# Performance work log

Measured on AMD Instinct MI355X. Metric: run time of the kernel, lower is better.

Reference implementation:

```python
import jax, jax.numpy as jnp
import numpy as np

HIDDEN = 512
HEADS = 8
HEAD_SIZE = HIDDEN // HEADS
INF = 10000.0


def _heads(x):
    # [N, L, D] -> [N, L, H, Dh]
    return x.reshape(x.shape[0], x.shape[1], HEADS, HEAD_SIZE)


def _alpha_from_logits(logits, mask_row, mask_col):
    # logits: [N, L1, L2, H]; mask_row: [N, L1]; mask_col: [N, L2]
    pair = (mask_row[:, :, None, None] * mask_col[:, None, :, None]) > 0  # [N,L1,L2,1]
    logits = jnp.where(pair, logits, logits - INF)
    alpha = jax.nn.softmax(logits, axis=2)
    row = (mask_row[:, :, None, None]) > 0  # [N,L1,1,1]
    return jnp.where(row, alpha, jnp.zeros_like(alpha))


def setup_inputs() -> dict:
    key = jax.random.key(0)
    ks = jax.random.split(key, 10)
    N, L1, L2, D = 4, 1024, 1024, HIDDEN
    input1 = jax.random.normal(ks[0], (N, L1, D), dtype=jnp.float32)
    input2 = jax.random.normal(ks[1], (N, L2, D), dtype=jnp.float32)
    # masks: 1 for valid tokens, with some padding at the tail
    mask1 = (jnp.arange(L1)[None, :] < jnp.array([L1, L1 - 64, L1 - 128, L1 - 200])[:, None]).astype(jnp.float32)
    mask2 = (jnp.arange(L2)[None, :] < jnp.array([L2 - 32, L2, L2 - 96, L2 - 10])[:, None]).astype(jnp.float32)
    s = 1.0 / np.sqrt(D)
    Wq1 = jax.random.normal(ks[2], (D, D), dtype=jnp.float32) * s
    Wk1 = jax.random.normal(ks[3], (D, D), dtype=jnp.float32) * s
    Wv1 = jax.random.normal(ks[4], (D, D), dtype=jnp.float32) * s
    Wq2 = jax.random.normal(ks[5], (D, D), dtype=jnp.float32) * s
    Wk2 = jax.random.normal(ks[6], (D, D), dtype=jnp.float32) * s
    Wv2 = jax.random.normal(ks[7], (D, D), dtype=jnp.float32) * s
    return {"input1": input1, "mask1": mask1, "input2": input2, "mask2": mask2,
            "Wq1": Wq1, "Wk1": Wk1, "Wv1": Wv1, "Wq2": Wq2, "Wk2": Wk2, "Wv2": Wv2}


def reference(input1, mask1, input2, mask2, Wq1, Wk1, Wv1, Wq2, Wk2, Wv2):
    # nn.Linear(bias=False): x @ W.T
    q1 = _heads(input1 @ Wq1.T)
    k1 = _heads(input1 @ Wk1.T)
    v1 = _heads(input1 @ Wv1.T)
    q2 = _heads(input2 @ Wq2.T)
    k2 = _heads(input2 @ Wk2.T)
    v2 = _heads(input2 @ Wv2.T)
    logits11 = jnp.einsum('blhd,bkhd->blkh', q1, k1)
    logits12 = jnp.einsum('blhd,bkhd->blkh', q1, k2)
    logits21 = jnp.einsum('blhd,bkhd->blkh', q2, k1)
    logits22 = jnp.einsum('blhd,bkhd->blkh', q2, k2)
    a11 = _alpha_from_logits(logits11, mask1, mask1)
    a12 = _alpha_from_logits(logits12, mask1, mask2)
    a21 = _alpha_from_logits(logits21, mask2, mask1)
    a22 = _alpha_from_logits(logits22, mask2, mask2)
    N, L1 = input1.shape[0], input1.shape[1]
    L2 = input2.shape[1]
    o11 = jnp.einsum('blkh,bkhd->blhd', a11, v1).reshape(N, L1, HIDDEN)
    o12 = jnp.einsum('blkh,bkhd->blhd', a12, v2).reshape(N, L1, HIDDEN)
    o21 = jnp.einsum('blkh,bkhd->blhd', a21, v1).reshape(N, L2, HIDDEN)
    o22 = jnp.einsum('blkh,bkhd->blhd', a22, v2).reshape(N, L2, HIDDEN)
    output1 = (o11 + o12) / 2
    output2 = (o21 + o22) / 2
    return (output1, output2)
```

## Files before the change

### kernel.cpp

```cpp
#include <hip/hip_runtime.h>

#define DEV static __device__ __forceinline__

typedef unsigned short u16;
typedef short bf16x8 __attribute__((ext_vector_type(8)));
typedef u16 u16x8v __attribute__((ext_vector_type(8)));
typedef u16 u16x4v __attribute__((ext_vector_type(4)));
typedef float f32x4 __attribute__((ext_vector_type(4)));

static constexpr int NB = 4, L = 1024, D = 512, H = 8, DH = 64;
static constexpr size_t E  = (size_t)NB * L * D;
static constexpr size_t WE = (size_t)D * D;

static constexpr size_t OFF_X1H = 0;
static constexpr size_t OFF_X1L = OFF_X1H + E;
static constexpr size_t OFF_X2H = OFF_X1L + E;
static constexpr size_t OFF_X2L = OFF_X2H + E;
static constexpr size_t OFF_WH  = OFF_X2L + E;
static constexpr size_t OFF_WL  = OFF_WH + 6 * WE;
static constexpr size_t OFF_QKV = OFF_WL + 6 * WE;
static constexpr size_t OFF_VLEN = OFF_QKV + 10 * E;

DEV u16 f2bf(float x) {
    unsigned u = __builtin_bit_cast(unsigned, x);
    unsigned r = u + 0x7FFFu + ((u >> 16) & 1u);
    return (u16)(r >> 16);
}
DEV float bf2f(u16 h) {
    unsigned u = ((unsigned)h) << 16;
    return __builtin_bit_cast(float, u);
}
DEV unsigned cvtpk(float lo, float hi) {
    unsigned r;
    asm("v_cvt_pk_bf16_f32 %0, %1, %2" : "=v"(r) : "v"(lo), "v"(hi));
    return r;
}
DEV bf16x8 ldfrag(const u16* p) {
    u16x8v t = *reinterpret_cast<const u16x8v*>(p);
    return __builtin_bit_cast(bf16x8, t);
}
typedef __attribute__((address_space(1))) const unsigned gas_u32;
typedef __attribute__((address_space(3))) unsigned las_u32;
DEV void gld16(const u16* g, u16* l) {
    __builtin_amdgcn_global_load_lds((gas_u32*)g, (las_u32*)l, 16, 0, 0);
}

__global__ __launch_bounds__(256) void k_split_all(const float* __restrict__ x1,
                                                   const float* __restrict__ x2,
                                                   const float* w0, const float* w1,
                                                   const float* w2, const float* w3,
                                                   const float* w4, const float* w5,
                                                   u16* __restrict__ ws) {
    int b = blockIdx.x;
    const float* src;
    u16 *hi, *lo;
    int i0;
    if (b < 2048)      { src = x1; hi = ws + OFF_X1H; lo = ws + OFF_X1L; i0 = b; }
    else if (b < 4096) { src = x2; hi = ws + OFF_X2H; lo = ws + OFF_X2L; i0 = b - 2048; }
    else {
        int wi = (b - 4096) >> 8;
        const float* wp[6] = {w0, w1, w2, w3, w4, w5};
        src = wp[wi];
        hi = ws + OFF_WH + (size_t)wi * WE;
        lo = ws + OFF_WL + (size_t)wi * WE;
        i0 = (b - 4096) & 255;
    }
    int i = i0 * 256 + threadIdx.x;
    float4 v = reinterpret_cast<const float4*>(src)[i];
    float xs[4] = {v.x, v.y, v.z, v.w};
    u16x4v h, l;
#pragma unroll
    for (int j = 0; j < 4; j++) {
        u16 hh = f2bf(xs[j]);
        h[j] = hh;
        l[j] = f2bf(xs[j] - bf2f(hh));
    }
    int idx = i * 4;
    int m = idx >> 9, e = idx & 511;
    int o = (m << 9) | (e ^ ((m & 7) << 3));
    *reinterpret_cast<u16x4v*>(hi + o) = h;
    *reinterpret_cast<u16x4v*>(lo + o) = l;
}

__global__ __launch_bounds__(256) void k_vlen(const float* __restrict__ m1,
                                              const float* __restrict__ m2,
                                              int* __restrict__ vl) {
    int b = blockIdx.x;
    int s = b >> 2, n = b & 3;
    const float* m = (s ? m2 : m1) + n * L;
    float p = 0.f;
    for (int i = threadIdx.x; i < L; i += 256) p += m[i];
#pragma unroll
    for (int mk = 1; mk < 64; mk <<= 1) p += __shfl_xor(p, mk, 64);
    __shared__ float w4[4];
    if ((threadIdx.x & 63) == 0) w4[threadIdx.x >> 6] = p;
    __syncthreads();
    if (threadIdx.x == 0) vl[b] = (int)(w4[0] + w4[1] + w4[2] + w4[3] + 0.5f);
}

__global__ __launch_bounds__(256) void k_proj(u16* __restrict__ ws) {
    __shared__ __align__(16) u16 ta[2][128][64];
    __shared__ __align__(16) u16 tb[2][128][64];

    const int b     = blockIdx.x;
    const int proj  = b >> 7;
    const int rem   = b & 127;
    const int mtile = rem >> 2;
    const int ntile = rem & 3;
    const int tid   = threadIdx.x;
    const int w     = tid >> 6;
    const int lane  = tid & 63;
    const int lr    = lane & 15;
    const int g     = lane >> 4;
    const int wr    = w >> 1, wc = w & 1;

    const int src  = proj / 3;
    const int kind = proj % 3;
    const u16* Xh = ws + (src ? OFF_X2H : OFF_X1H);
    const u16* Xl = ws + (src ? OFF_X2L : OFF_X1L);
    const u16* Wh = ws + OFF_WH + (size_t)proj * WE;
    const u16* Wl = ws + OFF_WL + (size_t)proj * WE;

    const int m0 = mtile * 128, n0 = ntile * 128;

    const int lrow = lane >> 3, lcol = lane & 7;
    const u16* gA0 = Xh + (size_t)(m0 + w * 32 + lrow) * 512 + lcol * 8;
    const u16* gA1 = Xl + (size_t)(m0 + w * 32 + lrow) * 512 + lcol * 8;
    const u16* gB0 = Wh + (size_t)(n0 + w * 32 + lrow) * 512 + lcol * 8;
    const u16* gB1 = Wl + (size_t)(n0 + w * 32 + lrow) * 512 + lcol * 8;

    f32x4 acc[4][4];
#pragma unroll
    for (int fr = 0; fr < 4; fr++)
#pragma unroll
        for (int cb = 0; cb < 4; cb++) acc[fr][cb] = {0.f, 0.f, 0.f, 0.f};

#pragma unroll 1
    for (int step = 0; step < 8; step++) {
        __syncthreads();
#pragma unroll
        for (int i = 0; i < 4; i++) {
            const int roff = w * 32 + i * 8;
            const int e0 = step * 64;
            gld16(gA0 + e0 + i * (8 * 512), &ta[0][roff][0]);
            gld16(gA1 + e0 + i * (8 * 512), &ta[1][roff][0]);
            gld16(gB0 + e0 + i * (8 * 512), &tb[0][roff][0]);
            gld16(gB1 + e0 + i * (8 * 512), &tb[1][roff][0]);
        }
        __syncthreads();

#pragma unroll
        for (int ks = 0; ks < 2; ks++) {
            bf16x8 ah[4], al[4];
#pragma unroll
            for (int fr = 0; fr < 4; fr++) {
                const int row = wr * 64 + fr * 16 + lr;
                const int ch = (ks * 4 + g) ^ (row & 7);
                ah[fr] = ldfrag(&ta[0][row][ch * 8]);
                al[fr] = ldfrag(&ta[1][row][ch * 8]);
            }
#pragma unroll
            for (int cb = 0; cb < 4; cb++) {
                const int rowb = wc * 64 + cb * 16 + lr;
                const int chb = (ks * 4 + g) ^ (rowb & 7);
                bf16x8 bh = ldfrag(&tb[0][rowb][chb * 8]);
                bf16x8 bl = ldfrag(&tb[1][rowb][chb * 8]);
#pragma unroll
                for (int fr = 0; fr < 4; fr++) {
                    acc[fr][cb] = __builtin_amdgcn_mfma_f32_16x16x32_bf16(ah[fr], bh, acc[fr][cb], 0, 0, 0);
                    acc[fr][cb] = __builtin_amdgcn_mfma_f32_16x16x32_bf16(ah[fr], bl, acc[fr][cb], 0, 0, 0);
                    acc[fr][cb] = __builtin_amdgcn_mfma_f32_16x16x32_bf16(al[fr], bh, acc[fr][cb], 0, 0, 0);
                }
            }
        }
    }

    if (kind < 2) {
        const float qscale = (kind == 0) ? 1.4426950408889634f : 1.0f;
        u16* dhi = ws + OFF_QKV + (size_t)(src * 4 + kind * 2) * E;
        u16* dlo = dhi + E;
#pragma unroll
        for (int fr = 0; fr < 4; fr++)
#pragma unroll
            for (int cb = 0; cb < 4; cb++) {
                int d  = n0 + wc * 64 + cb * 16 + lr;
                int hh = d >> 6, dh = d & 63;
#pragma unroll
                for (int r = 0; r < 4; r++) {
                    int m = m0 + wr * 64 + fr * 16 + g * 4 + r;
                    int n = m >> 10, li = m & 1023;
                    int dhs = kind ? (dh ^ ((li & 7) << 3)) : dh;
                    size_t idx = ((size_t)(n * H + hh) * L + li) * DH + dhs;
                    float v = acc[fr][cb][r] * qscale;
                    u16 hv = f2bf(v);
                    dhi[idx] = hv;
                    dlo[idx] = f2bf(v - bf2f(hv));
                }
            }
    } else {
        u16* vt = ws + OFF_QKV + (size_t)(8 + src) * E;
#pragma unroll
        for (int fr = 0; fr < 4; fr++)
#pragma unroll
            for (int cb = 0; cb < 4; cb++) {
                int d  = n0 + wc * 64 + cb * 16 + lr;
                int hh = d >> 6, dh = d & 63;
                int m  = m0 + wr * 64 + fr * 16 + g * 4;
                int n  = m >> 10, li = m & 1023;
                int lis = li ^ (((dh >> 2) & 3) << 3);
                u16x4v pk;
#pragma unroll
                for (int r = 0; r < 4; r++) pk[r] = f2bf(acc[fr][cb][r]);
                *reinterpret_cast<u16x4v*>(vt + ((size_t)(n * H + hh) * DH + dh) * L + lis) = pk;
            }
    }
}

__global__ __launch_bounds__(512, 2) void k_attn(const u16* __restrict__ ws,
                                                 float* __restrict__ out) {
    __shared__ __align__(16) u16 kbuf[2][2][2][32][64];
    __shared__ __align__(16) u16 vbuf[2][2][64][32];
    __shared__ __align__(16) u16 plds[8][2][16][32];

    const int bid  = blockIdx.x;
    const int b    = ((bid & 7) << 6) | (bid >> 3);
    const int oi   = b >> 8;
    const int n    = (b >> 6) & 3;
    const int hh   = (b >> 3) & 7;
    const int qt   = b & 7;
    const int tid  = threadIdx.x;
    const int w    = tid >> 6;
    const int s    = w >> 2;
    const int wq   = w & 3;
    const int lane = tid & 63;
    const int lr   = lane & 15;
    const int g    = lane >> 4;
    const int swz  = ((lr >> 1) & 7) << 2;
    const int tsw  = (lr >> 2) & 3;

    const size_t nh = (size_t)(n * H + hh);
    const u16* Qh = ws + OFF_QKV + (size_t)(oi * 4) * E;
    const int* vl = (const int*)(ws + OFF_VLEN);
    const int vls = vl[s * 4 + n];
    const int vlo = vl[oi * 4 + n];

    const int l0 = qt * 128 + wq * 32;
    bf16x8 qh[2][2];
#pragma unroll
    for (int rt = 0; rt < 2; rt++) {
        const size_t qb = (nh * L + l0 + rt * 16 + lr) * DH + g * 8;
        qh[rt][0] = ldfrag(Qh + qb);      qh[rt][1] = ldfrag(Qh + qb + 32);
    }

    float lrun[2] = {0.f, 0.f};
    f32x4 oacc[2][4];
#pragma unroll
    for (int rt = 0; rt < 2; rt++)
#pragma unroll
        for (int d = 0; d < 4; d++) oacc[rt][d] = {0.f, 0.f, 0.f, 0.f};

    const int nkt0 = (vl[n] + 31) >> 5;
    const int nkt1 = (vl[4 + n] + 31) >> 5;
    const int mykt = s ? nkt1 : nkt0;
    const int nktmax = nkt0 > nkt1 ? nkt0 : nkt1;

    const u16* gsrc[3];
    u16* ldst[3];
    int ginc[3], lstr[3];
#pragma unroll
    for (int i = 0; i < 3; i++) {
        const int c  = w * 3 + i;
        const int cs = c / 12, cr = c % 12;
        if (cr < 8) {
            const int hl = cr >> 2, rr = cr & 3;
            const u16* K = ws + OFF_QKV + (size_t)(2 + cs * 4 + hl) * E;
            gsrc[i] = K + (nh * L + rr * 8 + (lane >> 3)) * DH + (lane & 7) * 8;
            ldst[i] = &kbuf[0][cs][hl][rr * 8][0];
            ginc[i] = 32 * DH;
            lstr[i] = 2 * 2 * 32 * 64;
        } else {
            const int rr = cr - 8;
            const u16* V = ws + OFF_QKV + (size_t)(8 + cs) * E;
            gsrc[i] = V + (nh * DH + rr * 16 + (lane >> 2)) * L + (lane & 3) * 8;
            ldst[i] = &vbuf[0][cs][rr * 16][0];
            ginc[i] = 32;
            lstr[i] = 2 * 64 * 32;
        }
    }

#pragma unroll
    for (int i = 0; i < 3; i++) { gld16(gsrc[i], ldst[i]); gsrc[i] += ginc[i]; }
    __syncthreads();

    int cur = 0;
    const int srcb = (lane & 48) + ((lane >> 4) << 2);

#pragma unroll 1
    for (int kt = 0; kt < nktmax; kt++) {
        if (kt + 1 < nktmax) {
            const int nb = cur ^ 1;
#pragma unroll
            for (int i = 0; i < 3; i++) { gld16(gsrc[i], ldst[i] + nb * lstr[i]); gsrc[i] += ginc[i]; }
        }

        if (kt < mykt) {
            __builtin_amdgcn_s_setprio(1);
            f32x4 sfr[2][2];
#pragma unroll
            for (int j = 0; j < 2; j++) {
                const int row = j * 16 + lr;
                const int t0 = g ^ (row & 7);
                const int t1 = (g + 4) ^ (row & 7);
                bf16x8 kh0 = ldfrag(&kbuf[cur][s][0][row][t0 * 8]);
                bf16x8 kh1 = ldfrag(&kbuf[cur][s][0][row][t1 * 8]);
                bf16x8 kl0 = ldfrag(&kbuf[cur][s][1][row][t0 * 8]);
                bf16x8 kl1 = ldfrag(&kbuf[cur][s][1][row][t1 * 8]);
#pragma unroll
                for (int rt = 0; rt < 2; rt++) {
                    f32x4 a = {0.f, 0.f, 0.f, 0.f};
                    a = __builtin_amdgcn_mfma_f32_16x16x32_bf16(kh0, qh[rt][0], a, 0, 0, 0);
                    a = __builtin_amdgcn_mfma_f32_16x16x32_bf16(kh1, qh[rt][1], a, 0, 0, 0);
                    a = __builtin_amdgcn_mfma_f32_16x16x32_bf16(kl0, qh[rt][0], a, 0, 0, 0);
                    a = __builtin_amdgcn_mfma_f32_16x16x32_bf16(kl1, qh[rt][1], a, 0, 0, 0);
                    sfr[rt][j] = a;
                }
            }
            __builtin_amdgcn_s_setprio(0);
            if ((kt << 5) + 32 > vls) {
                const int kb0 = (kt << 5) + g * 4;
#pragma unroll
                for (int rt = 0; rt < 2; rt++)
#pragma unroll
                    for (int j = 0; j < 2; j++)
#pragma unroll
                        for (int r = 0; r < 4; r++)
                            if (kb0 + j * 16 + r >= vls) sfr[rt][j][r] = -1e30f;
            }
#pragma unroll
            for (int rt = 0; rt < 2; rt++) {
                float ps = 0.f;
#pragma unroll
                for (int j = 0; j < 2; j++) {
                    float e0 = __builtin_amdgcn_exp2f(sfr[rt][j][0]);
                    float e1 = __builtin_amdgcn_exp2f(sfr[rt][j][1]);
                    float e2 = __builtin_amdgcn_exp2f(sfr[rt][j][2]);
                    float e3 = __builtin_amdgcn_exp2f(sfr[rt][j][3]);
                    ps += (e0 + e1) + (e2 + e3);
                    uint2 pk;
                    pk.x = cvtpk(e0, e1);
                    pk.y = cvtpk(e2, e3);
                    *reinterpret_cast<uint2*>(&plds[w][rt][lr][(j * 16 + g * 4) ^ swz]) = pk;
                }
                lrun[rt] += ps;
            }
            bf16x8 pa[2];
#pragma unroll
            for (int rt = 0; rt < 2; rt++) {
                u16x4v p0 = *reinterpret_cast<const u16x4v*>(&plds[w][rt][lr][(g * 8) ^ swz]);
                u16x4v p1 = *reinterpret_cast<const u16x4v*>(&plds[w][rt][lr][(g * 8 + 4) ^ swz]);
                u16x8v pt;
#pragma unroll
                for (int i = 0; i < 4; i++) { pt[i] = p0[i]; pt[i + 4] = p1[i]; }
                pa[rt] = __builtin_bit_cast(bf16x8, pt);
            }
            const int t = g ^ tsw;
            __builtin_amdgcn_s_setprio(1);
#pragma unroll
            for (int d = 0; d < 4; d++) {
                const int dh = d * 16 + lr;
                bf16x8 v8 = ldfrag(&vbuf[cur][s][dh][t * 8]);
                oacc[0][d] = __builtin_amdgcn_mfma_f32_16x16x32_bf16(pa[0], v8, oacc[0][d], 0, 0, 0);
                oacc[1][d] = __builtin_amdgcn_mfma_f32_16x16x32_bf16(pa[1], v8, oacc[1][d], 0, 0, 0);
            }
            __builtin_amdgcn_s_setprio(0);
        }
        __syncthreads();
        cur ^= 1;
    }

    float ofin[2][4][4];
#pragma unroll
    for (int rt = 0; rt < 2; rt++) {
        lrun[rt] += __shfl_xor(lrun[rt], 16, 64);
        lrun[rt] += __shfl_xor(lrun[rt], 32, 64);
#pragma unroll
        for (int r = 0; r < 4; r++) {
            float lq = __shfl(lrun[rt], srcb + r, 64);
            float inv = __builtin_amdgcn_rcpf(lq);
#pragma unroll
            for (int d = 0; d < 4; d++) ofin[rt][d][r] = oacc[rt][d][r] * inv;
        }
    }

    float (*comb)[32][64] = (float(*)[32][64])&kbuf[0][0][0][0][0];
    if (s == 0) {
#pragma unroll
        for (int rt = 0; rt < 2; rt++)
#pragma unroll
            for (int d = 0; d < 4; d++)
#pragma unroll
                for (int r = 0; r < 4; r++)
                    comb[wq][rt * 16 + g * 4 + r][d * 16 + lr] = ofin[rt][d][r];
    }
    __syncthreads();
    if (s == 1) {
        float* ob = out + (size_t)oi * ((size_t)NB * L * D);
#pragma unroll
        for (int rt = 0; rt < 2; rt++)
#pragma unroll
            for (int r = 0; r < 4; r++) {
                int row = l0 + rt * 16 + g * 4 + r;
#pragma unroll
                for (int d = 0; d < 4; d++) {
                    float v = 0.5f * (ofin[rt][d][r] + comb[wq][rt * 16 + g * 4 + r][d * 16 + lr]);
                    v = (row < vlo) ? v : 0.f;
                    ob[((size_t)n * L + row) * D + hh * DH + d * 16 + lr] = v;
                }
            }
    }
}

extern "C" void kernel_launch(void* const* d_in, const int* in_sizes, int n_in,
                              void* d_out, int out_size, void* d_ws, size_t ws_size,
                              hipStream_t stream) {
    const float* input1 = (const float*)d_in[0];
    const float* mask1  = (const float*)d_in[1];
    const float* input2 = (const float*)d_in[2];
    const float* mask2  = (const float*)d_in[3];
    u16*   ws  = (u16*)d_ws;
    float* out = (float*)d_out;

    k_split_all<<<5632, 256, 0, stream>>>(input1, input2,
                                          (const float*)d_in[4], (const float*)d_in[5],
                                          (const float*)d_in[6], (const float*)d_in[7],
                                          (const float*)d_in[8], (const float*)d_in[9], ws);
    k_vlen<<<8, 256, 0, stream>>>(mask1, mask2, (int*)(ws + OFF_VLEN));
    k_proj<<<768, 256, 0, stream>>>(ws);
    k_attn<<<512, 512, 0, stream>>>(ws, out);
}
```

Before: 111.1 us.

## Double-buffer projection GEMM LDS tiles with 32-wide K steps and new swizzle

The projection GEMM now splits K into 16 steps of 32 and uses two LDS buffers, so global-to-LDS loads for the next step are issued before the MFMAs on the current step. This replaces the old load-sync-compute pattern, which had two barriers per step, with one barrier per step. The XOR swizzle is changed to a 4-chunk pattern based on (row>>1)&3 to fit the narrower 32-element rows, and the conversion kernel's swizzle is updated to match. The cost is smaller K tiles, meaning more loop iterations, and an LDS footprint that stays at 64KB because the buffer is double-buffered.

New measurement: 119.9 us. 1.08x slower.

```diff
diff --git a/kernel.cpp b/kernel.cpp
--- a/kernel.cpp
+++ b/kernel.cpp
@@ -77,7 +77,7 @@
     }
     int idx = i * 4;
     int m = idx >> 9, e = idx & 511;
-    int o = (m << 9) | (e ^ ((m & 7) << 3));
+    int o = (m << 9) | (e ^ (((m >> 1) & 3) << 3));
     *reinterpret_cast<u16x4v*>(hi + o) = h;
     *reinterpret_cast<u16x4v*>(lo + o) = l;
 }
@@ -99,8 +99,7 @@
 }
 
 __global__ __launch_bounds__(256) void k_proj(u16* __restrict__ ws) {
-    __shared__ __align__(16) u16 ta[2][128][64];
-    __shared__ __align__(16) u16 tb[2][128][64];
+    __shared__ __align__(16) u16 tile[2][4][128][32];
 
     const int b     = blockIdx.x;
     const int proj  = b >> 7;
@@ -123,11 +122,20 @@
 
     const int m0 = mtile * 128, n0 = ntile * 128;
 
-    const int lrow = lane >> 3, lcol = lane & 7;
-    const u16* gA0 = Xh + (size_t)(m0 + w * 32 + lrow) * 512 + lcol * 8;
-    const u16* gA1 = Xl + (size_t)(m0 + w * 32 + lrow) * 512 + lcol * 8;
-    const u16* gB0 = Wh + (size_t)(n0 + w * 32 + lrow) * 512 + lcol * 8;
-    const u16* gB1 = Wl + (size_t)(n0 + w * 32 + lrow) * 512 + lcol * 8;
+    const u16* gpan[4] = {Xh + (size_t)m0 * 512, Xl + (size_t)m0 * 512,
+                          Wh + (size_t)n0 * 512, Wl + (size_t)n0 * 512};
+    u16* const tbase = &tile[0][0][0][0];
+    constexpr int DSTR = 4 * 128 * 32;
+    const u16* gsrc[8];
+    int loff[8];
+#pragma unroll
+    for (int i = 0; i < 8; i++) {
+        const int c = w * 8 + i;
+        const int pan = c >> 3, rr = c & 7;
+        const int row = rr * 16 + (lane >> 2);
+        gsrc[i] = gpan[pan] + (size_t)row * 512 + (lane & 3) * 8;
+        loff[i] = pan * (128 * 32) + rr * 16 * 32;
+    }
 
     f32x4 acc[4][4];
 #pragma unroll
@@ -135,44 +143,42 @@
 #pragma unroll
         for (int cb = 0; cb < 4; cb++) acc[fr][cb] = {0.f, 0.f, 0.f, 0.f};
 
+#pragma unroll
+    for (int i = 0; i < 8; i++) { gld16(gsrc[i], tbase + loff[i]); gsrc[i] += 32; }
+    __syncthreads();
+
+    int buf = 0;
 #pragma unroll 1
-    for (int step = 0; step < 8; step++) {
+    for (int step = 0; step < 16; step++) {
+        if (step + 1 < 16) {
+            const int nb = buf ^ 1;
+#pragma unroll
+            for (int i = 0; i < 8; i++) { gld16(gsrc[i], tbase + nb * DSTR + loff[i]); gsrc[i] += 32; }
+        }
+
+        bf16x8 ah[4], al[4];
+#pragma unroll
+        for (int fr = 0; fr < 4; fr++) {
+            const int row = wr * 64 + fr * 16 + lr;
+            const int ch = g ^ ((row >> 1) & 3);
+            ah[fr] = ldfrag(&tile[buf][0][row][ch * 8]);
+            al[fr] = ldfrag(&tile[buf][1][row][ch * 8]);
+        }
+#pragma unroll
+        for (int cb = 0; cb < 4; cb++) {
+            const int rowb = wc * 64 + cb * 16 + lr;
+            const int chb = g ^ ((rowb >> 1) & 3);
+            bf16x8 bh = ldfrag(&tile[buf][2][rowb][chb * 8]);
+            bf16x8 bl = ldfrag(&tile[buf][3][rowb][chb * 8]);
+#pragma unroll
+            for (int fr = 0; fr < 4; fr++) {
+                acc[fr][cb] = __builtin_amdgcn_mfma_f32_16x16x32_bf16(ah[fr], bh, acc[fr][cb], 0, 0, 0);
+                acc[fr][cb] = __builtin_amdgcn_mfma_f32_16x16x32_bf16(ah[fr], bl, acc[fr][cb], 0, 0, 0);
+                acc[fr][cb] = __builtin_amdgcn_mfma_f32_16x16x32_bf16(al[fr], bh, acc[fr][cb], 0, 0, 0);
+            }
+        }
         __syncthreads();
-#pragma unroll
-        for (int i = 0; i < 4; i++) {
-            const int roff = w * 32 + i * 8;
-            const int e0 = step * 64;
-            gld16(gA0 + e0 + i * (8 * 512), &ta[0][roff][0]);
-            gld16(gA1 + e0 + i * (8 * 512), &ta[1][roff][0]);
-            gld16(gB0 + e0 + i * (8 * 512), &tb[0][roff][0]);
-            gld16(gB1 + e0 + i * (8 * 512), &tb[1][roff][0]);
-        }
-        __syncthreads();
-
-#pragma unroll
-        for (int ks = 0; ks < 2; ks++) {
-            bf16x8 ah[4], al[4];
-#pragma unroll
-            for (int fr = 0; fr < 4; fr++) {
-                const int row = wr * 64 + fr * 16 + lr;
-                const int ch = (ks * 4 + g) ^ (row & 7);
-                ah[fr] = ldfrag(&ta[0][row][ch * 8]);
-                al[fr] = ldfrag(&ta[1][row][ch * 8]);
-            }
-#pragma unroll
-            for (int cb = 0; cb < 4; cb++) {
-                const int rowb = wc * 64 + cb * 16 + lr;
-                const int chb = (ks * 4 + g) ^ (rowb & 7);
-                bf16x8 bh = ldfrag(&tb[0][rowb][chb * 8]);
-                bf16x8 bl = ldfrag(&tb[1][rowb][chb * 8]);
-#pragma unroll
-                for (int fr = 0; fr < 4; fr++) {
-                    acc[fr][cb] = __builtin_amdgcn_mfma_f32_16x16x32_bf16(ah[fr], bh, acc[fr][cb], 0, 0, 0);
-                    acc[fr][cb] = __builtin_amdgcn_mfma_f32_16x16x32_bf16(ah[fr], bl, acc[fr][cb], 0, 0, 0);
-                    acc[fr][cb] = __builtin_amdgcn_mfma_f32_16x16x32_bf16(al[fr], bh, acc[fr][cb], 0, 0, 0);
-                }
-            }
-        }
+        buf ^= 1;
     }
 
     if (kind < 2) {
```
